# Kernel tuning notes

Measured on AMD Instinct MI355X. Metric: run time of the kernel, lower is better.

## Reference

```python
import jax, jax.numpy as jnp
import numpy as np

N, E, IN, H, D = 50000, 800000, 128, 4, 32
NEG_SLOPE = 0.2


def setup_inputs() -> dict:
    key = jax.random.key(0)
    ks = jax.random.split(key, 7)
    feat = jax.random.normal(ks[0], (N, IN), dtype=jnp.float32)
    src = jax.random.randint(ks[1], (E,), 0, N)
    dst = jax.random.randint(ks[2], (E,), 0, N)
    fc_w = jax.random.normal(ks[3], (H * D, IN), dtype=jnp.float32) * 0.05
    attn_l = jax.random.normal(ks[4], (H, D), dtype=jnp.float32) * 0.05
    attn_r = jax.random.normal(ks[5], (H, D), dtype=jnp.float32) * 0.05
    res_w = jax.random.normal(ks[6], (H * D, IN), dtype=jnp.float32) * 0.05
    return {"feat": feat, "src": src, "dst": dst, "fc_w": fc_w,
            "attn_l": attn_l, "attn_r": attn_r, "res_w": res_w}


def reference(feat, src, dst, fc_w, attn_l, attn_r, res_w):
    # Shared linear projection: [N, H, D]
    h = (feat @ fc_w.T).reshape(N, H, D)
    # Per-node attention logits: el (source side), er (destination side), [N, H]
    el = jnp.einsum("nhd,hd->nh", h, attn_l)
    er = jnp.einsum("nhd,hd->nh", h, attn_r)
    # Per-edge score and exp (original uses plain exp, no max-subtraction)
    e = jax.nn.leaky_relu(el[src] + er[dst], negative_slope=NEG_SLOPE)  # [E, H]
    coeff = jnp.exp(e)
    # Softmax denominator per destination node
    denom = jax.ops.segment_sum(coeff, dst, num_segments=N)  # [N, H]
    alpha = coeff / denom[dst]  # [E, H]
    # Weighted aggregation of source features into destinations: [N, H, D]
    msg = alpha[:, :, None] * h[src]  # [E, H, D]
    rst = jax.ops.segment_sum(msg, dst, num_segments=N)
    # Residual projection (always applied in this module)
    resval = (feat @ res_w.T).reshape(N, H, D)
    return rst + resval
```

## Files before the change

kernel.cpp:

```cpp
#include <hip/hip_runtime.h>
#include <hip/hip_bf16.h>

#define NN 50000
#define EE 800000
#define HH 4
#define HDIM 128

#define GEMM_BLOCKS ((NN + 63) / 64)
#define CNT_BLOCKS  ((EE + 255) / 256)
#define ELR_BLOCKS  ((NN * HH + 255) / 256)
#define SEG_BLOCKS  ((NN + 255) / 256)

typedef __attribute__((ext_vector_type(8))) short bf16x8;
typedef __attribute__((ext_vector_type(4))) float f32x4;

__device__ inline unsigned short f2bf(float f) {
    unsigned u = __float_as_uint(f);
    u = u + 0x7FFFu + ((u >> 16) & 1u);
    return (unsigned short)(u >> 16);
}
__device__ inline float bfl(unsigned u) { return __uint_as_float(u << 16); }
__device__ inline float bfh(unsigned u) { return __uint_as_float(u & 0xFFFF0000u); }

__global__ __launch_bounds__(256) void gemm_count_kernel(const float* __restrict__ feat,
                                                         const float* __restrict__ fc_w,
                                                         const float* __restrict__ res_w,
                                                         unsigned short* __restrict__ h16,
                                                         float* __restrict__ out,
                                                         const int* __restrict__ dst,
                                                         int* __restrict__ cnt,
                                                         unsigned short* __restrict__ rank16,
                                                         int n) {
    if (blockIdx.x >= GEMM_BLOCKS) {
        int ed = (blockIdx.x - GEMM_BLOCKS) * 256 + threadIdx.x;
        if (ed < EE) {
            int d = dst[ed];
            rank16[ed] = (unsigned short)atomicAdd(&cnt[d], 1);
        }
        return;
    }

    __shared__ unsigned short As[64][136];
    int t = threadIdx.x;
    int w = t >> 6;
    int l = t & 63;
    int l15 = l & 15;
    int kg = l >> 4;
    int r0 = blockIdx.x * 64;
    int colbase = w * 64;

    bf16x8 bfrag[4][4];
    #pragma unroll
    for (int ct = 0; ct < 4; ++ct) {
        int col = colbase + ct * 16 + l15;
        const float* wrow = (col < 128) ? &fc_w[(size_t)col * 128]
                                        : &res_w[(size_t)(col - 128) * 128];
        #pragma unroll
        for (int ks = 0; ks < 4; ++ks) {
            int k0 = ks * 32 + kg * 8;
            float4 b0 = *(const float4*)&wrow[k0];
            float4 b1 = *(const float4*)&wrow[k0 + 4];
            bf16x8 b;
            b[0] = (short)f2bf(b0.x); b[1] = (short)f2bf(b0.y);
            b[2] = (short)f2bf(b0.z); b[3] = (short)f2bf(b0.w);
            b[4] = (short)f2bf(b1.x); b[5] = (short)f2bf(b1.y);
            b[6] = (short)f2bf(b1.z); b[7] = (short)f2bf(b1.w);
            bfrag[ct][ks] = b;
        }
    }

    for (int i = t; i < 64 * 32; i += 256) {
        int r = i >> 5;
        int c4 = (i & 31) << 2;
        float4 v = make_float4(0.f, 0.f, 0.f, 0.f);
        if (r0 + r < n) v = *(const float4*)&feat[(size_t)(r0 + r) * 128 + c4];
        unsigned short tmp[4] = { f2bf(v.x), f2bf(v.y), f2bf(v.z), f2bf(v.w) };
        *(uint2*)&As[r][c4] = *(uint2*)tmp;
    }
    __syncthreads();

    f32x4 acc[4][4];
    #pragma unroll
    for (int rt = 0; rt < 4; ++rt)
        #pragma unroll
        for (int ct = 0; ct < 4; ++ct)
            acc[rt][ct] = (f32x4){0.f, 0.f, 0.f, 0.f};

    #pragma unroll
    for (int ks = 0; ks < 4; ++ks) {
        bf16x8 afrag[4];
        #pragma unroll
        for (int rt = 0; rt < 4; ++rt)
            afrag[rt] = *(const bf16x8*)&As[rt * 16 + l15][ks * 32 + kg * 8];
        #pragma unroll
        for (int rt = 0; rt < 4; ++rt)
            #pragma unroll
            for (int ct = 0; ct < 4; ++ct)
                acc[rt][ct] = __builtin_amdgcn_mfma_f32_16x16x32_bf16(
                    afrag[rt], bfrag[ct][ks], acc[rt][ct], 0, 0, 0);
    }

    int rb = 4 * kg;
    if (w < 2) {
        #pragma unroll
        for (int rt = 0; rt < 4; ++rt)
            #pragma unroll
            for (int ct = 0; ct < 4; ++ct)
                #pragma unroll
                for (int r = 0; r < 4; ++r) {
                    int row = r0 + rt * 16 + rb + r;
                    if (row < n)
                        h16[(size_t)row * 128 + colbase + ct * 16 + l15] = f2bf(acc[rt][ct][r]);
                }
    } else {
        #pragma unroll
        for (int rt = 0; rt < 4; ++rt)
            #pragma unroll
            for (int ct = 0; ct < 4; ++ct)
                #pragma unroll
                for (int r = 0; r < 4; ++r) {
                    int row = r0 + rt * 16 + rb + r;
                    if (row < n)
                        out[(size_t)row * 128 + (colbase - 128) + ct * 16 + l15] = acc[rt][ct][r];
                }
    }
}

__global__ void elr_seg_kernel(const unsigned short* __restrict__ h16,
                               const float* __restrict__ al,
                               const float* __restrict__ ar,
                               float* __restrict__ el,
                               float* __restrict__ er,
                               const int* __restrict__ cnt,
                               int* __restrict__ base,
                               int* __restrict__ total) {
    int bx = blockIdx.x;
    int t = threadIdx.x;
    if (bx < ELR_BLOCKS) {
        int idx = bx * 256 + t;
        if (idx >= NN * HH) return;
        int node = idx >> 2;
        int hh = idx & 3;
        const unsigned short* hp = &h16[(size_t)node * 128 + hh * 32];
        const float* alp = &al[hh * 32];
        const float* arp = &ar[hh * 32];
        float a = 0.f, b = 0.f;
        #pragma unroll
        for (int c = 0; c < 4; ++c) {
            uint4 hv = *(const uint4*)&hp[c * 8];
            unsigned uu[4] = { hv.x, hv.y, hv.z, hv.w };
            #pragma unroll
            for (int j = 0; j < 4; ++j) {
                float v0 = bfl(uu[j]);
                float v1 = bfh(uu[j]);
                int d = c * 8 + j * 2;
                a = fmaf(v0, alp[d], a);     a = fmaf(v1, alp[d + 1], a);
                b = fmaf(v0, arp[d], b);     b = fmaf(v1, arp[d + 1], b);
            }
        }
        el[idx] = a;
        er[idx] = b;
    } else {
        int idx = (bx - ELR_BLOCKS) * 256 + t;
        int lane = t & 63;
        int c = (idx < NN) ? cnt[idx] : 0;
        int pre = c;
        #pragma unroll
        for (int d = 1; d < 64; d <<= 1) {
            int v = __shfl_up(pre, d, 64);
            if (lane >= d) pre += v;
        }
        int wtot = __shfl(pre, 63, 64);
        int wbase = 0;
        if (lane == 63) wbase = atomicAdd(total, wtot);
        wbase = __shfl(wbase, 63, 64);
        if (idx < NN) base[idx] = wbase + pre - c;
    }
}

__global__ void place_kernel(const int* __restrict__ src,
                             const int* __restrict__ dst,
                             const int* __restrict__ base,
                             const unsigned short* __restrict__ rank16,
                             int* __restrict__ perm_src,
                             int e) {
    int ed = blockIdx.x * 256 + threadIdx.x;
    if (ed >= e) return;
    int d = dst[ed];
    int pos = base[d] + (int)rank16[ed];
    perm_src[pos] = src[ed];
}

__global__ __launch_bounds__(256) void gather_agg_kernel(const int* __restrict__ base,
                                                         const int* __restrict__ cnt,
                                                         const int* __restrict__ perm_src,
                                                         const float* __restrict__ el,
                                                         const float* __restrict__ er,
                                                         const unsigned short* __restrict__ h16,
                                                         float* __restrict__ out) {
    int t = threadIdx.x;
    int node = blockIdx.x * 8 + (t >> 5);
    int ln = t & 31;
    int d0 = ln << 2;
    int hh = ln >> 3;
    int q  = ln & 7;
    int o0 = base[node];
    int deg = cnt[node];
    int o1 = o0 + deg;
    float erh = er[node * 4 + hh];

    float dsum = 0.f;
    for (int j = o0 + q; j < o1; j += 8) {
        int s = perm_src[j];
        float x = el[s * 4 + hh] + erh;
        x = (x > 0.f) ? x : 0.2f * x;
        dsum += __expf(x);
    }
    dsum += __shfl_xor(dsum, 1, 64);
    dsum += __shfl_xor(dsum, 2, 64);
    dsum += __shfl_xor(dsum, 4, 64);
    float inv = (deg > 0) ? 1.0f / dsum : 0.f;

    size_t oidx = (size_t)node * 128 + d0;
    float4 acc = *(const float4*)&out[oidx];
    int j = o0;
    for (; j + 3 < o1; j += 4) {
        int s0 = perm_src[j];
        int s1 = perm_src[j + 1];
        int s2 = perm_src[j + 2];
        int s3 = perm_src[j + 3];
        float x0 = el[s0 * 4 + hh] + erh; x0 = (x0 > 0.f) ? x0 : 0.2f * x0;
        float x1 = el[s1 * 4 + hh] + erh; x1 = (x1 > 0.f) ? x1 : 0.2f * x1;
        float x2 = el[s2 * 4 + hh] + erh; x2 = (x2 > 0.f) ? x2 : 0.2f * x2;
        float x3 = el[s3 * 4 + hh] + erh; x3 = (x3 > 0.f) ? x3 : 0.2f * x3;
        float a0 = __expf(x0) * inv;
        float a1 = __expf(x1) * inv;
        float a2 = __expf(x2) * inv;
        float a3 = __expf(x3) * inv;
        uint2 h0 = *(const uint2*)&h16[(size_t)s0 * 128 + d0];
        uint2 h1 = *(const uint2*)&h16[(size_t)s1 * 128 + d0];
        uint2 h2 = *(const uint2*)&h16[(size_t)s2 * 128 + d0];
        uint2 h3 = *(const uint2*)&h16[(size_t)s3 * 128 + d0];
        acc.x = fmaf(a0, bfl(h0.x), acc.x); acc.y = fmaf(a0, bfh(h0.x), acc.y);
        acc.z = fmaf(a0, bfl(h0.y), acc.z); acc.w = fmaf(a0, bfh(h0.y), acc.w);
        acc.x = fmaf(a1, bfl(h1.x), acc.x); acc.y = fmaf(a1, bfh(h1.x), acc.y);
        acc.z = fmaf(a1, bfl(h1.y), acc.z); acc.w = fmaf(a1, bfh(h1.y), acc.w);
        acc.x = fmaf(a2, bfl(h2.x), acc.x); acc.y = fmaf(a2, bfh(h2.x), acc.y);
        acc.z = fmaf(a2, bfl(h2.y), acc.z); acc.w = fmaf(a2, bfh(h2.y), acc.w);
        acc.x = fmaf(a3, bfl(h3.x), acc.x); acc.y = fmaf(a3, bfh(h3.x), acc.y);
        acc.z = fmaf(a3, bfl(h3.y), acc.z); acc.w = fmaf(a3, bfh(h3.y), acc.w);
    }
    for (; j < o1; ++j) {
        int s0 = perm_src[j];
        float x0 = el[s0 * 4 + hh] + erh; x0 = (x0 > 0.f) ? x0 : 0.2f * x0;
        float a0 = __expf(x0) * inv;
        uint2 h0 = *(const uint2*)&h16[(size_t)s0 * 128 + d0];
        acc.x = fmaf(a0, bfl(h0.x), acc.x); acc.y = fmaf(a0, bfh(h0.x), acc.y);
        acc.z = fmaf(a0, bfl(h0.y), acc.z); acc.w = fmaf(a0, bfh(h0.y), acc.w);
    }
    *(float4*)&out[oidx] = acc;
}

extern "C" void kernel_launch(void* const* d_in, const int* in_sizes, int n_in,
                              void* d_out, int out_size, void* d_ws, size_t ws_size,
                              hipStream_t stream) {
    const float* feat   = (const float*)d_in[0];
    const int*   src    = (const int*)d_in[1];
    const int*   dst    = (const int*)d_in[2];
    const float* fc_w   = (const float*)d_in[3];
    const float* attn_l = (const float*)d_in[4];
    const float* attn_r = (const float*)d_in[5];
    const float* res_w  = (const float*)d_in[6];
    float* out = (float*)d_out;

    unsigned short* h16 = (unsigned short*)d_ws;
    float* el  = (float*)(h16 + (size_t)NN * HDIM);
    float* er  = el + (size_t)NN * HH;
    int*   perm_src = (int*)(er + (size_t)NN * HH);
    unsigned short* rank16 = (unsigned short*)(perm_src + EE);
    int*   cnt    = (int*)(rank16 + EE);
    int*   total  = cnt + NN;
    int*   base   = total + 1;

    hipMemsetAsync(cnt, 0, (size_t)(NN + 1) * sizeof(int), stream);

    gemm_count_kernel<<<GEMM_BLOCKS + CNT_BLOCKS, 256, 0, stream>>>(
        feat, fc_w, res_w, h16, out, dst, cnt, rank16, NN);

    elr_seg_kernel<<<ELR_BLOCKS + SEG_BLOCKS, 256, 0, stream>>>(
        h16, attn_l, attn_r, el, er, cnt, base, total);

    place_kernel<<<CNT_BLOCKS, 256, 0, stream>>>(src, dst, base, rank16, perm_src, EE);

    gather_agg_kernel<<<NN / 8, 256, 0, stream>>>(base, cnt, perm_src, el, er, h16, out);
}
```

Measured before the change: 134.5 us.

## Fuse softmax denominator into aggregation loop and split count from GEMM kernel

The aggregation kernel no longer makes a separate pass over each node's incoming edges to compute the softmax denominator. It accumulates unnormalized exp-weighted features and the denominator in the same loop, then scales once at the end before adding the residual. This removes a second round of perm_src and el gathers per node. Separately, the edge-counting atomics are moved out of the fused GEMM kernel into their own launch, which adds a launch but gives the GEMM kernel a uniform grid.

```diff
diff --git a/kernel.cpp b/kernel.cpp
--- a/kernel.cpp
+++ b/kernel.cpp
@@ -22,24 +22,22 @@
 __device__ inline float bfl(unsigned u) { return __uint_as_float(u << 16); }
 __device__ inline float bfh(unsigned u) { return __uint_as_float(u & 0xFFFF0000u); }
 
-__global__ __launch_bounds__(256) void gemm_count_kernel(const float* __restrict__ feat,
-                                                         const float* __restrict__ fc_w,
-                                                         const float* __restrict__ res_w,
-                                                         unsigned short* __restrict__ h16,
-                                                         float* __restrict__ out,
-                                                         const int* __restrict__ dst,
-                                                         int* __restrict__ cnt,
-                                                         unsigned short* __restrict__ rank16,
-                                                         int n) {
-    if (blockIdx.x >= GEMM_BLOCKS) {
-        int ed = (blockIdx.x - GEMM_BLOCKS) * 256 + threadIdx.x;
-        if (ed < EE) {
-            int d = dst[ed];
-            rank16[ed] = (unsigned short)atomicAdd(&cnt[d], 1);
-        }
-        return;
-    }
-
+__global__ void count_kernel(const int* __restrict__ dst,
+                             int* __restrict__ cnt,
+                             unsigned short* __restrict__ rank16,
+                             int e) {
+    int ed = blockIdx.x * 256 + threadIdx.x;
+    if (ed >= e) return;
+    int d = dst[ed];
+    rank16[ed] = (unsigned short)atomicAdd(&cnt[d], 1);
+}
+
+__global__ __launch_bounds__(256) void mfma_gemm_kernel(const float* __restrict__ feat,
+                                                        const float* __restrict__ fc_w,
+                                                        const float* __restrict__ res_w,
+                                                        unsigned short* __restrict__ h16,
+                                                        float* __restrict__ out,
+                                                        int n) {
     __shared__ unsigned short As[64][136];
     int t = threadIdx.x;
     int w = t >> 6;
@@ -203,26 +201,13 @@
     int ln = t & 31;
     int d0 = ln << 2;
     int hh = ln >> 3;
-    int q  = ln & 7;
     int o0 = base[node];
     int deg = cnt[node];
     int o1 = o0 + deg;
     float erh = er[node * 4 + hh];
 
+    float4 acc = make_float4(0.f, 0.f, 0.f, 0.f);
     float dsum = 0.f;
-    for (int j = o0 + q; j < o1; j += 8) {
-        int s = perm_src[j];
-        float x = el[s * 4 + hh] + erh;
-        x = (x > 0.f) ? x : 0.2f * x;
-        dsum += __expf(x);
-    }
-    dsum += __shfl_xor(dsum, 1, 64);
-    dsum += __shfl_xor(dsum, 2, 64);
-    dsum += __shfl_xor(dsum, 4, 64);
-    float inv = (deg > 0) ? 1.0f / dsum : 0.f;
-
-    size_t oidx = (size_t)node * 128 + d0;
-    float4 acc = *(const float4*)&out[oidx];
     int j = o0;
     for (; j + 3 < o1; j += 4) {
         int s0 = perm_src[j];
@@ -233,32 +218,41 @@
         float x1 = el[s1 * 4 + hh] + erh; x1 = (x1 > 0.f) ? x1 : 0.2f * x1;
         float x2 = el[s2 * 4 + hh] + erh; x2 = (x2 > 0.f) ? x2 : 0.2f * x2;
         float x3 = el[s3 * 4 + hh] + erh; x3 = (x3 > 0.f) ? x3 : 0.2f * x3;
-        float a0 = __expf(x0) * inv;
-        float a1 = __expf(x1) * inv;
-        float a2 = __expf(x2) * inv;
-        float a3 = __expf(x3) * inv;
+        float c0 = __expf(x0);
+        float c1 = __expf(x1);
+        float c2 = __expf(x2);
+        float c3 = __expf(x3);
+        dsum += (c0 + c1) + (c2 + c3);
         uint2 h0 = *(const uint2*)&h16[(size_t)s0 * 128 + d0];
         uint2 h1 = *(const uint2*)&h16[(size_t)s1 * 128 + d0];
         uint2 h2 = *(const uint2*)&h16[(size_t)s2 * 128 + d0];
         uint2 h3 = *(const uint2*)&h16[(size_t)s3 * 128 + d0];
-        acc.x = fmaf(a0, bfl(h0.x), acc.x); acc.y = fmaf(a0, bfh(h0.x), acc.y);
-        acc.z = fmaf(a0, bfl(h0.y), acc.z); acc.w = fmaf(a0, bfh(h0.y), acc.w);
-        acc.x = fmaf(a1, bfl(h1.x), acc.x); acc.y = fmaf(a1, bfh(h1.x), acc.y);
-        acc.z = fmaf(a1, bfl(h1.y), acc.z); acc.w = fmaf(a1, bfh(h1.y), acc.w);
-        acc.x = fmaf(a2, bfl(h2.x), acc.x); acc.y = fmaf(a2, bfh(h2.x), acc.y);
-        acc.z = fmaf(a2, bfl(h2.y), acc.z); acc.w = fmaf(a2, bfh(h2.y), acc.w);
-        acc.x = fmaf(a3, bfl(h3.x), acc.x); acc.y = fmaf(a3, bfh(h3.x), acc.y);
-        acc.z = fmaf(a3, bfl(h3.y), acc.z); acc.w = fmaf(a3, bfh(h3.y), acc.w);
+        acc.x = fmaf(c0, bfl(h0.x), acc.x); acc.y = fmaf(c0, bfh(h0.x), acc.y);
+        acc.z = fmaf(c0, bfl(h0.y), acc.z); acc.w = fmaf(c0, bfh(h0.y), acc.w);
+        acc.x = fmaf(c1, bfl(h1.x), acc.x); acc.y = fmaf(c1, bfh(h1.x), acc.y);
+        acc.z = fmaf(c1, bfl(h1.y), acc.z); acc.w = fmaf(c1, bfh(h1.y), acc.w);
+        acc.x = fmaf(c2, bfl(h2.x), acc.x); acc.y = fmaf(c2, bfh(h2.x), acc.y);
+        acc.z = fmaf(c2, bfl(h2.y), acc.z); acc.w = fmaf(c2, bfh(h2.y), acc.w);
+        acc.x = fmaf(c3, bfl(h3.x), acc.x); acc.y = fmaf(c3, bfh(h3.x), acc.y);
+        acc.z = fmaf(c3, bfl(h3.y), acc.z); acc.w = fmaf(c3, bfh(h3.y), acc.w);
     }
     for (; j < o1; ++j) {
         int s0 = perm_src[j];
         float x0 = el[s0 * 4 + hh] + erh; x0 = (x0 > 0.f) ? x0 : 0.2f * x0;
-        float a0 = __expf(x0) * inv;
+        float c0 = __expf(x0);
+        dsum += c0;
         uint2 h0 = *(const uint2*)&h16[(size_t)s0 * 128 + d0];
-        acc.x = fmaf(a0, bfl(h0.x), acc.x); acc.y = fmaf(a0, bfh(h0.x), acc.y);
-        acc.z = fmaf(a0, bfl(h0.y), acc.z); acc.w = fmaf(a0, bfh(h0.y), acc.w);
-    }
-    *(float4*)&out[oidx] = acc;
+        acc.x = fmaf(c0, bfl(h0.x), acc.x); acc.y = fmaf(c0, bfh(h0.x), acc.y);
+        acc.z = fmaf(c0, bfl(h0.y), acc.z); acc.w = fmaf(c0, bfh(h0.y), acc.w);
+    }
+    float inv = (deg > 0) ? 1.0f / dsum : 0.f;
+    size_t oidx = (size_t)node * 128 + d0;
+    float4 res = *(const float4*)&out[oidx];
+    res.x = fmaf(acc.x, inv, res.x);
+    res.y = fmaf(acc.y, inv, res.y);
+    res.z = fmaf(acc.z, inv, res.z);
+    res.w = fmaf(acc.w, inv, res.w);
+    *(float4*)&out[oidx] = res;
 }
 
 extern "C" void kernel_launch(void* const* d_in, const int* in_sizes, int n_in,
@@ -284,8 +278,9 @@
 
     hipMemsetAsync(cnt, 0, (size_t)(NN + 1) * sizeof(int), stream);
 
-    gemm_count_kernel<<<GEMM_BLOCKS + CNT_BLOCKS, 256, 0, stream>>>(
-        feat, fc_w, res_w, h16, out, dst, cnt, rank16, NN);
+    count_kernel<<<CNT_BLOCKS, 256, 0, stream>>>(dst, cnt, rank16, EE);
+
+    mfma_gemm_kernel<<<GEMM_BLOCKS, 256, 0, stream>>>(feat, fc_w, res_w, h16, out, NN);
 
     elr_seg_kernel<<<ELR_BLOCKS + SEG_BLOCKS, 256, 0, stream>>>(
         h16, attn_l, attn_r, el, er, cnt, base, total);
```

Result: slower. 142.1 us (+5.6%).
